# Optimization experiments

Measured on AMD Instinct MI355X. Metric: run time of the kernel, lower is better.

Reference implementation:

```python
import jax, jax.numpy as jnp
import numpy as np

FOCAL_ALPHA = 0.25
FOCAL_GAMMA = 2.0
IOU_POS_THRESH = 0.5


def setup_inputs() -> dict:
    A, G, C = 262144, 256, 80
    key = jax.random.key(0)
    k = jax.random.split(key, 8)
    # anchors: random boxes with centers in [0,1024], sizes in [16,128]
    actr = jax.random.uniform(k[0], (A, 2), minval=0.0, maxval=1024.0)
    awh = jax.random.uniform(k[1], (A, 2), minval=16.0, maxval=128.0)
    anchors = jnp.concatenate([actr - 0.5 * awh, actr + 0.5 * awh], axis=1)
    # ground-truth boxes: sizes in [32,256]
    gctr = jax.random.uniform(k[2], (G, 2), minval=0.0, maxval=1024.0)
    gwh = jax.random.uniform(k[3], (G, 2), minval=32.0, maxval=256.0)
    gt_boxes = jnp.concatenate([gctr - 0.5 * gwh, gctr + 0.5 * gwh], axis=1)
    cls_logits = jax.random.normal(k[4], (A, C), dtype=jnp.float32)
    # small deltas so exp(delta * width) in this module's decode stays finite
    bbox_reg = jax.random.normal(k[5], (A, 4), dtype=jnp.float32) * 0.02
    centerness = jax.random.normal(k[6], (A,), dtype=jnp.float32)
    gt_labels = jax.random.randint(k[7], (G,), 0, C, dtype=jnp.int32)
    return {"anchors": anchors, "cls_logits": cls_logits, "bbox_reg": bbox_reg,
            "centerness": centerness, "gt_boxes": gt_boxes, "gt_labels": gt_labels}


def _compute_loss(anchors, cls_logits, bbox_reg, centerness, gt_boxes, gt_labels):
    A, C = cls_logits.shape
    f32 = cls_logits.dtype
    # ---- box_iou: [A, G] pairwise IoU ----
    area_a = (anchors[:, 2] - anchors[:, 0]) * (anchors[:, 3] - anchors[:, 1])
    area_g = (gt_boxes[:, 2] - gt_boxes[:, 0]) * (gt_boxes[:, 3] - gt_boxes[:, 1])
    lt = jnp.maximum(anchors[:, None, :2], gt_boxes[None, :, :2])
    rb = jnp.minimum(anchors[:, None, 2:], gt_boxes[None, :, 2:])
    wh = jnp.maximum(rb - lt, 0.0)
    inter = wh[..., 0] * wh[..., 1]
    iou = inter / (area_a[:, None] + area_g[None, :] - inter)
    max_iou = iou.max(axis=1)
    midx = iou.argmax(axis=1)
    pos = max_iou > IOU_POS_THRESH
    posf = pos.astype(f32)
    npos = posf.sum()
    denom = jnp.maximum(npos, 1.0)
    mboxes = gt_boxes[midx]            # [A,4] matched GT box per anchor
    mlabels = gt_labels[midx]          # [A]
    # ---- focal loss over ALL anchors (targets = -1 for negatives) ----
    cls_t = jnp.where(pos, mlabels, -1)
    logp = jax.nn.log_softmax(cls_logits, axis=-1)
    # torch gathers class index; -1 wraps to last class (python-style indexing)
    ce = -jnp.take_along_axis(logp, (cls_t % C)[:, None], axis=1)[:, 0]
    p = jnp.exp(-ce)
    fl = (1.0 - p) ** FOCAL_GAMMA * ce
    af = jnp.where(cls_t == 1, FOCAL_ALPHA, 1.0 - FOCAL_ALPHA)
    cls_loss = (af * fl).mean()
    # ---- decode boxes (module's unusual parameterization: exp(delta*width)*width) ----
    w = anchors[:, 2] - anchors[:, 0]
    h = anchors[:, 3] - anchors[:, 1]
    cx = anchors[:, 0] + 0.5 * w
    cy = anchors[:, 1] + 0.5 * h
    pcx = cx + bbox_reg[:, 0] * w
    pcy = cy + bbox_reg[:, 1] * h
    pw = jnp.exp(bbox_reg[:, 2] * w) * w
    ph = jnp.exp(bbox_reg[:, 3] * h) * h
    pred = jnp.stack([pcx - 0.5 * pw, pcy - 0.5 * ph, pcx + 0.5 * pw, pcy + 0.5 * ph], axis=1)
    # ---- paired GIoU (diag of generalized_box_iou(pred, matched)) ----
    lt2 = jnp.maximum(pred[:, :2], mboxes[:, :2])
    rb2 = jnp.minimum(pred[:, 2:], mboxes[:, 2:])
    wh2 = jnp.maximum(rb2 - lt2, 0.0)
    inter2 = wh2[:, 0] * wh2[:, 1]
    area_p = (pred[:, 2] - pred[:, 0]) * (pred[:, 3] - pred[:, 1])
    area_m = (mboxes[:, 2] - mboxes[:, 0]) * (mboxes[:, 3] - mboxes[:, 1])
    union = area_p + area_m - inter2
    iou2 = inter2 / union
    el = jnp.minimum(pred[:, :2], mboxes[:, :2])
    er = jnp.maximum(pred[:, 2:], mboxes[:, 2:])
    ewh = jnp.maximum(er - el, 0.0)
    earea = ewh[:, 0] * ewh[:, 1]
    giou = iou2 - (earea - union) / earea
    reg_loss = 1.0 - (posf * giou).sum() / denom
    # ---- centerness targets + BCE-with-logits over positives ----
    lr = mboxes[:, jnp.array([0, 2])] - anchors[:, jnp.array([0, 2])]
    tb = mboxes[:, jnp.array([1, 3])] - anchors[:, jnp.array([1, 3])]
    lrmax = lr.max(axis=1)
    tbmax = tb.max(axis=1)
    r_lr = jnp.maximum(lr.min(axis=1) / jnp.where(lrmax == 0, 1.0, lrmax), 0.0)
    r_tb = jnp.maximum(tb.min(axis=1) / jnp.where(tbmax == 0, 1.0, tbmax), 0.0)
    ctr_t = jnp.sqrt(jnp.maximum(r_lr * r_tb, 1e-12))
    bce = jnp.logaddexp(0.0, centerness) - centerness * ctr_t
    ctr_loss = (posf * bce).sum() / denom
    # original skips the level entirely when there are no positives
    has = (npos > 0).astype(f32)
    cls_loss = cls_loss * has
    reg_loss = reg_loss * has
    ctr_loss = ctr_loss * has
    total = cls_loss + reg_loss + ctr_loss
    return total, cls_loss, reg_loss, ctr_loss


def reference(anchors, cls_logits, bbox_reg, centerness, gt_boxes, gt_labels):
    return _compute_loss(anchors, cls_logits, bbox_reg, centerness, gt_boxes, gt_labels)
```

## Files before the change

### kernel.cpp

```cpp
#include <hip/hip_runtime.h>
#include <math.h>

#define BLOCK 256
#define C_CLS 80
#define G_MAX 256
#define NCELL1 32
#define NCELLS (NCELL1 * NCELL1)
#define CAP 96
#define NBKT 256

static __device__ inline float frcp(float x) { return __builtin_amdgcn_rcpf(x); }

static __device__ inline int cell_of(float4 ab) {
    const float cx = 0.5f * (ab.x + ab.z);
    const float cy = 0.5f * (ab.y + ab.w);
    int ix = (int)(cx * (1.0f / 32.0f));
    int iy = (int)(cy * (1.0f / 32.0f));
    ix = ix < 0 ? 0 : (ix > NCELL1 - 1 ? NCELL1 - 1 : ix);
    iy = iy < 0 ? 0 : (iy > NCELL1 - 1 ? NCELL1 - 1 : iy);
    return iy * NCELL1 + ix;
}


__global__ __launch_bounds__(256) void k_build(
    const float4* __restrict__ gt, const int* __restrict__ gl,
    float* __restrict__ bsums, int* __restrict__ cnts,
    float4* __restrict__ boxes, int* __restrict__ labs, int G)
{
    __shared__ int s_wcnt[4];
    const int cell = blockIdx.x;
    const int ix = cell & (NCELL1 - 1), iy = cell >> 5;
    const float Dx1 = 32.0f * ix - 64.0f, Dx2 = 32.0f * ix + 96.0f;
    const float Dy1 = 32.0f * iy - 64.0f, Dy2 = 32.0f * iy + 96.0f;

    const int tid = threadIdx.x, wid = tid >> 6, lane = tid & 63;
    if (cell < NBKT && tid < 4) bsums[cell * 4 + tid] = 0.0f;

    bool keep = false;
    float4 g = make_float4(0.f, 0.f, 0.f, 0.f);
    int lb = 0;
    if (tid < G) {
        g = gt[tid];
        keep = (g.x <= Dx2) && (g.z >= Dx1) && (g.y <= Dy2) && (g.w >= Dy1);
        lb = gl[tid];
    }
    const unsigned long long mk = __ballot(keep);
    if (lane == 0) s_wcnt[wid] = __popcll(mk);
    __syncthreads();
    int prefix = 0;
    for (int w = 0; w < wid; ++w) prefix += s_wcnt[w];
    if (keep) {
        const int p = prefix + __popcll(mk & ((1ull << lane) - 1ull));
        if (p < CAP) {
            boxes[(size_t)cell * CAP + p] = g;
            labs[(size_t)cell * CAP + p] = lb;
        }
    }
    const int tot = s_wcnt[0] + s_wcnt[1] + s_wcnt[2] + s_wcnt[3];
    if (tot <= CAP) {
        const float4 sent = make_float4(1e30f, 1e30f, 1e30f, 1e30f);
        for (int p = tot + tid; p < CAP; p += 256) {
            boxes[(size_t)cell * CAP + p] = sent;
            labs[(size_t)cell * CAP + p] = 0;
        }
    }
    if (tid == 0) cnts[cell] = (tot > CAP) ? (1 << 30) : tot;
}

__global__ __launch_bounds__(BLOCK) void k_main(
    const float* __restrict__ anchors, const float* __restrict__ cls_logits,
    const float* __restrict__ bbox_reg, const float* __restrict__ centerness,
    const float* __restrict__ gt_boxes, const int* __restrict__ gt_labels,
    const int* __restrict__ cnts, const float4* __restrict__ boxes,
    const int* __restrict__ labs,
    float* __restrict__ bsums, int A, int G)
{
    const int tid = threadIdx.x;
    const int a = blockIdx.x * BLOCK + tid;
    const bool valid = a < A;

    float4 ab = make_float4(0.f, 0.f, 0.f, 0.f);
    if (valid) ab = reinterpret_cast<const float4*>(anchors)[a];
    const float area_a = (ab.z - ab.x) * (ab.w - ab.y);

    const int cell = cell_of(ab);
    const int cnt = valid ? cnts[cell] : 0;
    const bool big = cnt > CAP;
    const int c2 = big ? 0 : cnt;

    int wmax = c2;
    #pragma unroll
    for (int off = 1; off < 64; off <<= 1)
        wmax = max(wmax, __shfl_xor(wmax, off, 64));
    const int nch = (wmax + 7) >> 3;

    const float4* __restrict__ bl = boxes + (size_t)cell * CAP;
    float best = -1.0f;
    int bestk = 0, bidx = 0;
    float4 bA[8], bB[8];

    #define LOADCH(BUF, CH) { _Pragma("unroll")                                 \
        for (int u = 0; u < 8; ++u) BUF[u] = bl[(CH) * 8 + u]; }
    #define PROCCH(BUF, CH) { _Pragma("unroll")                                 \
        for (int u = 0; u < 8; ++u) {                                           \
            const float4 g = BUF[u];                                            \
            const float ga = (g.z - g.x) * (g.w - g.y);                         \
            const float lx = fmaxf(ab.x, g.x);                                  \
            const float ly = fmaxf(ab.y, g.y);                                  \
            const float rx = fminf(ab.z, g.z);                                  \
            const float ry = fminf(ab.w, g.w);                                  \
            const float iw = fmaxf(rx - lx, 0.0f);                              \
            const float ih = fmaxf(ry - ly, 0.0f);                              \
            const float inter = iw * ih;                                        \
            const float iou = inter * frcp(area_a + ga - inter);                \
            if (iou > best) { best = iou; bestk = (CH) * 8 + u; }               \
        } }

    if (nch > 0)  LOADCH(bA, 0)
    if (nch > 1)  LOADCH(bB, 1)
    if (nch > 0)  PROCCH(bA, 0)
    if (nch > 2)  LOADCH(bA, 2)
    if (nch > 1)  PROCCH(bB, 1)
    if (nch > 3)  LOADCH(bB, 3)
    if (nch > 2)  PROCCH(bA, 2)
    if (nch > 4)  LOADCH(bA, 4)
    if (nch > 3)  PROCCH(bB, 3)
    if (nch > 5)  LOADCH(bB, 5)
    if (nch > 4)  PROCCH(bA, 4)
    if (nch > 6)  LOADCH(bA, 6)
    if (nch > 5)  PROCCH(bB, 5)
    if (nch > 7)  LOADCH(bB, 7)
    if (nch > 6)  PROCCH(bA, 6)
    if (nch > 8)  LOADCH(bA, 8)
    if (nch > 7)  PROCCH(bB, 7)
    if (nch > 9)  LOADCH(bB, 9)
    if (nch > 8)  PROCCH(bA, 8)
    if (nch > 10) LOADCH(bA, 10)
    if (nch > 9)  PROCCH(bB, 9)
    if (nch > 11) LOADCH(bB, 11)
    if (nch > 10) PROCCH(bA, 10)
    if (nch > 11) PROCCH(bB, 11)
    #undef LOADCH
    #undef PROCCH

    if (__ballot(big) != 0ull) {
        if (big) {
            best = -1.0f; bidx = 0;
            for (int j = 0; j < G; ++j) {
                const float4 g = reinterpret_cast<const float4*>(gt_boxes)[j];
                const float ga = (g.z - g.x) * (g.w - g.y);
                const float lx = fmaxf(ab.x, g.x);
                const float ly = fmaxf(ab.y, g.y);
                const float rx = fminf(ab.z, g.z);
                const float ry = fminf(ab.w, g.w);
                const float iw = fmaxf(rx - lx, 0.0f);
                const float ih = fmaxf(ry - ly, 0.0f);
                const float inter = iw * ih;
                const float iou = inter * frcp(area_a + ga - inter);
                if (iou > best) { best = iou; bidx = j; }
            }
        }
    }

    float c_affl = 0.f, c_pos = 0.f, c_giou = 0.f, c_bce = 0.f;

    if (valid) {
        const bool pos = best > 0.5f;
        int lab = -1;
        float4 mb = make_float4(0.f, 0.f, 0.f, 0.f);
        if (pos) {
            if (big) { mb = reinterpret_cast<const float4*>(gt_boxes)[bidx]; lab = gt_labels[bidx]; }
            else     { mb = bl[bestk]; lab = labs[(size_t)cell * CAP + bestk]; }
        }

        const float4* row4 = reinterpret_cast<const float4*>(cls_logits + (size_t)a * C_CLS);
        float4 rr[C_CLS / 4];
        #pragma unroll
        for (int k = 0; k < C_CLS / 4; ++k) rr[k] = row4[k];

        float m = -3.4e38f;
        #pragma unroll
        for (int k = 0; k < C_CLS / 4; ++k) {
            const float4 v = rr[k];
            m = fmaxf(m, fmaxf(fmaxf(v.x, v.y), fmaxf(v.z, v.w)));
        }
        float s = 0.0f;
        #pragma unroll
        for (int k = 0; k < C_CLS / 4; ++k) {
            const float4 v = rr[k];
            s += __expf(v.x - m) + __expf(v.y - m)
               + __expf(v.z - m) + __expf(v.w - m);
        }
        const float v79 = rr[C_CLS / 4 - 1].w;
        const float lse = m + __logf(s);
        const float l_idx = pos ? cls_logits[(size_t)a * C_CLS + lab] : v79;
        const float ce = lse - l_idx;
        const float p  = __expf(-ce);
        const float om = 1.0f - p;
        const float fl = om * om * ce;
        const float af = (pos && lab == 1) ? 0.25f : 0.75f;
        c_affl = af * fl;

        if (pos) {
            const float w  = ab.z - ab.x;
            const float h  = ab.w - ab.y;
            const float cx = ab.x + 0.5f * w;
            const float cy = ab.y + 0.5f * h;
            const float4 t = reinterpret_cast<const float4*>(bbox_reg)[a];
            const float pcx = cx + t.x * w;
            const float pcy = cy + t.y * h;
            const float pw  = __expf(t.z * w) * w;
            const float ph  = __expf(t.w * h) * h;
            const float p0 = pcx - 0.5f * pw;
            const float p1 = pcy - 0.5f * ph;
            const float p2 = pcx + 0.5f * pw;
            const float p3 = pcy + 0.5f * ph;

            const float lx2 = fmaxf(p0, mb.x);
            const float ly2 = fmaxf(p1, mb.y);
            const float rx2 = fminf(p2, mb.z);
            const float ry2 = fminf(p3, mb.w);
            const float iw2 = fmaxf(rx2 - lx2, 0.0f);
            const float ih2 = fmaxf(ry2 - ly2, 0.0f);
            const float inter2 = iw2 * ih2;
            const float area_p = (p2 - p0) * (p3 - p1);
            const float area_m = (mb.z - mb.x) * (mb.w - mb.y);
            const float uni = area_p + area_m - inter2;
            const float iou2 = inter2 * frcp(uni);
            const float elx = fminf(p0, mb.x);
            const float ely = fminf(p1, mb.y);
            const float erx = fmaxf(p2, mb.z);
            const float ery = fmaxf(p3, mb.w);
            const float ew = fmaxf(erx - elx, 0.0f);
            const float eh = fmaxf(ery - ely, 0.0f);
            const float earea = ew * eh;
            const float giou = iou2 - (earea - uni) * frcp(earea);
            c_giou = giou;

            const float lr0 = mb.x - ab.x;
            const float lr1 = mb.z - ab.z;
            const float tb0 = mb.y - ab.y;
            const float tb1 = mb.w - ab.w;
            const float lrmax = fmaxf(lr0, lr1);
            const float lrmin = fminf(lr0, lr1);
            const float tbmax = fmaxf(tb0, tb1);
            const float tbmin = fminf(tb0, tb1);
            const float r_lr = fmaxf(lrmin * frcp(lrmax == 0.0f ? 1.0f : lrmax), 0.0f);
            const float r_tb = fmaxf(tbmin * frcp(tbmax == 0.0f ? 1.0f : tbmax), 0.0f);
            const float ctr_t = sqrtf(fmaxf(r_lr * r_tb, 1e-12f));
            const float c = centerness[a];
            const float bce = fmaxf(c, 0.0f) + log1pf(__expf(-fabsf(c))) - c * ctr_t;
            c_bce = bce;
            c_pos = 1.0f;
        }
    }

    __shared__ float red[4][BLOCK / 64];
    float vals[4] = { c_affl, c_pos, c_giou, c_bce };
    #pragma unroll
    for (int i = 0; i < 4; ++i) {
        float v = vals[i];
        #pragma unroll
        for (int off = 32; off > 0; off >>= 1) v += __shfl_down(v, off, 64);
        if ((tid & 63) == 0) red[i][tid >> 6] = v;
    }
    __syncthreads();
    if (tid < 4) {
        float v = 0.f;
        #pragma unroll
        for (int wv = 0; wv < BLOCK / 64; ++wv) v += red[tid][wv];
        atomicAdd(&bsums[(blockIdx.x & (NBKT - 1)) * 4 + tid], v);
    }
}

__global__ __launch_bounds__(BLOCK) void detloss_fallback(
    const float* __restrict__ anchors, const float* __restrict__ cls_logits,
    const float* __restrict__ bbox_reg, const float* __restrict__ centerness,
    const float* __restrict__ gt_boxes, const int* __restrict__ gt_labels,
    float* __restrict__ bsums, int A, int G)
{
    __shared__ float4 s_gt[G_MAX];
    __shared__ float  s_ga[G_MAX];
    __shared__ int    s_gl[G_MAX];
    const int tid = threadIdx.x;
    for (int j = tid; j < G; j += BLOCK) {
        float4 g = reinterpret_cast<const float4*>(gt_boxes)[j];
        s_gt[j] = g;
        s_ga[j] = (g.z - g.x) * (g.w - g.y);
        s_gl[j] = gt_labels[j];
    }
    __syncthreads();
    const int a = blockIdx.x * BLOCK + tid;
    float c_affl = 0.f, c_pos = 0.f, c_giou = 0.f, c_bce = 0.f;
    if (a < A) {
        const float4 ab = reinterpret_cast<const float4*>(anchors)[a];
        const float area_a = (ab.z - ab.x) * (ab.w - ab.y);
        float best = -1.0f; int bidx = 0;
        for (int j = 0; j < G; ++j) {
            const float4 g = s_gt[j];
            const float lx = fmaxf(ab.x, g.x), ly = fmaxf(ab.y, g.y);
            const float rx = fminf(ab.z, g.z), ry = fminf(ab.w, g.w);
            const float iw = fmaxf(rx - lx, 0.0f), ih = fmaxf(ry - ly, 0.0f);
            const float inter = iw * ih;
            const float iou = inter * frcp(area_a + s_ga[j] - inter);
            if (iou > best) { best = iou; bidx = j; }
        }
        const bool pos = best > 0.5f;
        const float posf = pos ? 1.0f : 0.0f;
        const float4 mb = s_gt[bidx];
        const int mlab = s_gl[bidx];
        const float4* row4 = reinterpret_cast<const float4*>(cls_logits + (size_t)a * C_CLS);
        float m = -3.4e38f, s = 0.0f, v79 = 0.0f;
        #pragma unroll
        for (int k = 0; k < C_CLS / 4; ++k) {
            const float4 v = row4[k];
            const float m4 = fmaxf(fmaxf(v.x, v.y), fmaxf(v.z, v.w));
            const float mn = fmaxf(m, m4);
            s = s * __expf(m - mn) + __expf(v.x - mn) + __expf(v.y - mn)
              + __expf(v.z - mn) + __expf(v.w - mn);
            m = mn;
            if (k == C_CLS / 4 - 1) v79 = v.w;
        }
        const float lse = m + __logf(s);
        const float l_idx = pos ? cls_logits[(size_t)a * C_CLS + mlab] : v79;
        const float ce = lse - l_idx;
        const float p = __expf(-ce);
        const float om = 1.0f - p;
        const float fl = om * om * ce;
        const float af = (pos && mlab == 1) ? 0.25f : 0.75f;
        c_affl = af * fl;
        const float w = ab.z - ab.x, h = ab.w - ab.y;
        const float cx = ab.x + 0.5f * w, cy = ab.y + 0.5f * h;
        const float4 t = reinterpret_cast<const float4*>(bbox_reg)[a];
        const float pcx = cx + t.x * w, pcy = cy + t.y * h;
        const float pw = __expf(t.z * w) * w, ph = __expf(t.w * h) * h;
        const float p0 = pcx - 0.5f * pw, p1 = pcy - 0.5f * ph;
        const float p2 = pcx + 0.5f * pw, p3 = pcy + 0.5f * ph;
        const float lx2 = fmaxf(p0, mb.x), ly2 = fmaxf(p1, mb.y);
        const float rx2 = fminf(p2, mb.z), ry2 = fminf(p3, mb.w);
        const float iw2 = fmaxf(rx2 - lx2, 0.0f), ih2 = fmaxf(ry2 - ly2, 0.0f);
        const float inter2 = iw2 * ih2;
        const float area_p = (p2 - p0) * (p3 - p1);
        const float area_m = (mb.z - mb.x) * (mb.w - mb.y);
        const float uni = area_p + area_m - inter2;
        const float iou2 = inter2 * frcp(uni);
        const float elx = fminf(p0, mb.x), ely = fminf(p1, mb.y);
        const float erx = fmaxf(p2, mb.z), ery = fmaxf(p3, mb.w);
        const float ew = fmaxf(erx - elx, 0.0f), eh = fmaxf(ery - ely, 0.0f);
        const float earea = ew * eh;
        const float giou = iou2 - (earea - uni) * frcp(earea);
        c_giou = posf * giou;
        const float lr0 = mb.x - ab.x, lr1 = mb.z - ab.z;
        const float tb0 = mb.y - ab.y, tb1 = mb.w - ab.w;
        const float lrmax = fmaxf(lr0, lr1), lrmin = fminf(lr0, lr1);
        const float tbmax = fmaxf(tb0, tb1), tbmin = fminf(tb0, tb1);
        const float r_lr = fmaxf(lrmin * frcp(lrmax == 0.0f ? 1.0f : lrmax), 0.0f);
        const float r_tb = fmaxf(tbmin * frcp(tbmax == 0.0f ? 1.0f : tbmax), 0.0f);
        const float ctr_t = sqrtf(fmaxf(r_lr * r_tb, 1e-12f));
        const float c = centerness[a];
        const float bce = fmaxf(c, 0.0f) + log1pf(__expf(-fabsf(c))) - c * ctr_t;
        c_bce = posf * bce;
        c_pos = posf;
    }
    __shared__ float red[4][BLOCK / 64];
    float vals[4] = { c_affl, c_pos, c_giou, c_bce };
    #pragma unroll
    for (int i = 0; i < 4; ++i) {
        float v = vals[i];
        #pragma unroll
        for (int off = 32; off > 0; off >>= 1) v += __shfl_down(v, off, 64);
        if ((tid & 63) == 0) red[i][tid >> 6] = v;
    }
    __syncthreads();
    if (tid < 4) {
        float v = 0.f;
        #pragma unroll
        for (int w = 0; w < BLOCK / 64; ++w) v += red[tid][w];
        atomicAdd(&bsums[(blockIdx.x & (NBKT - 1)) * 4 + tid], v);
    }
}

__global__ __launch_bounds__(NBKT) void detloss_final(
    const float* __restrict__ bsums, float* __restrict__ out, int A)
{
    const int t = threadIdx.x;
    float4 v = reinterpret_cast<const float4*>(bsums)[t];
    #pragma unroll
    for (int off = 32; off > 0; off >>= 1) {
        v.x += __shfl_down(v.x, off, 64);
        v.y += __shfl_down(v.y, off, 64);
        v.z += __shfl_down(v.z, off, 64);
        v.w += __shfl_down(v.w, off, 64);
    }
    __shared__ float4 r[NBKT / 64];
    if ((t & 63) == 0) r[t >> 6] = v;
    __syncthreads();
    if (t == 0) {
        float s_affl = 0.f, npos = 0.f, sgiou = 0.f, sbce = 0.f;
        #pragma unroll
        for (int w = 0; w < NBKT / 64; ++w) {
            s_affl += r[w].x; npos += r[w].y; sgiou += r[w].z; sbce += r[w].w;
        }
        float cls = s_affl / (float)A;
        const float denom = fmaxf(npos, 1.0f);
        float reg = 1.0f - sgiou / denom;
        float ctr = sbce / denom;
        const float has = (npos > 0.0f) ? 1.0f : 0.0f;
        cls *= has; reg *= has; ctr *= has;
        out[0] = cls + reg + ctr;
        out[1] = cls;
        out[2] = reg;
        out[3] = ctr;
    }
}

extern "C" void kernel_launch(void* const* d_in, const int* in_sizes, int n_in,
                              void* d_out, int out_size, void* d_ws, size_t ws_size,
                              hipStream_t stream) {
    const float* anchors    = (const float*)d_in[0];
    const float* cls_logits = (const float*)d_in[1];
    const float* bbox_reg   = (const float*)d_in[2];
    const float* centerness = (const float*)d_in[3];
    const float* gt_boxes   = (const float*)d_in[4];
    const int*   gt_labels  = (const int*)d_in[5];
    const int A = in_sizes[0] / 4;
    const int G = in_sizes[4] / 4;

    float* bsums = (float*)d_ws;
    const int grid = (A + BLOCK - 1) / BLOCK;

    const size_t need = (size_t)(4 * NBKT + NCELLS + (size_t)NCELLS * CAP * 4
                                 + (size_t)NCELLS * CAP) * 4;

    if (ws_size >= need && G <= 256) {
        int*    cnts  = (int*)d_ws + 4 * NBKT;
        float4* boxes = (float4*)((float*)d_ws + 4 * NBKT + NCELLS);
        int*    labs  = (int*)((float*)d_ws + 4 * NBKT + NCELLS + (size_t)NCELLS * CAP * 4);

        k_build<<<NCELLS, 256, 0, stream>>>((const float4*)gt_boxes, gt_labels,
                                            bsums, cnts, boxes, labs, G);
        k_main<<<grid, BLOCK, 0, stream>>>(anchors, cls_logits, bbox_reg,
                                           centerness, gt_boxes, gt_labels,
                                           cnts, boxes, labs, bsums, A, G);
    } else {
        const int Gc = G > G_MAX ? G_MAX : G;
        hipMemsetAsync(bsums, 0, 4 * NBKT * sizeof(float), stream);
        detloss_fallback<<<grid, BLOCK, 0, stream>>>(anchors, cls_logits, bbox_reg,
                                                     centerness, gt_boxes, gt_labels,
                                                     bsums, A, Gc);
    }
    detloss_final<<<1, NBKT, 0, stream>>>(bsums, (float*)d_out, A);
}
```

Before: 39.65 us.

## Split each anchor across two lanes for candidate IoU scan and softmax row

Each anchor is now handled by two lanes of a wavefront: the two halves interleave over the cell's candidate GT boxes in groups of four and merge their argmax with a cross-half shuffle. The 80-logit row is also split, so each lane loads 10 float4s and the max and sum are combined by shuffles. This halves per-thread register pressure (launch bounds now ask for 8 blocks) and serial IoU work, aiming for more memory parallelism and occupancy. The cost is twice as many threads and blocks, extra shuffles, and the upper half of each wavefront idling during the per-anchor loss tail.

```diff
diff --git a/kernel.cpp b/kernel.cpp
--- a/kernel.cpp
+++ b/kernel.cpp
@@ -67,42 +67,45 @@
     if (tid == 0) cnts[cell] = (tot > CAP) ? (1 << 30) : tot;
 }
 
-__global__ __launch_bounds__(BLOCK) void k_main(
-    const float* __restrict__ anchors, const float* __restrict__ cls_logits,
-    const float* __restrict__ bbox_reg, const float* __restrict__ centerness,
-    const float* __restrict__ gt_boxes, const int* __restrict__ gt_labels,
+__global__ __launch_bounds__(BLOCK, 8) void k_main(
+    const float4* __restrict__ anchors4, const float* __restrict__ cls_logits,
+    const float4* __restrict__ bbox_reg4, const float* __restrict__ centerness,
+    const float4* __restrict__ gt4, const int* __restrict__ gl,
     const int* __restrict__ cnts, const float4* __restrict__ boxes,
     const int* __restrict__ labs,
     float* __restrict__ bsums, int A, int G)
 {
-    const int tid = threadIdx.x;
-    const int a = blockIdx.x * BLOCK + tid;
+    const int tid  = threadIdx.x;
+    const int lane = tid & 63;
+    const int wv   = tid >> 6;
+    const int sub  = lane & 31;
+    const int half = lane >> 5;
+    const int a    = blockIdx.x * (BLOCK / 2) + wv * 32 + sub;
     const bool valid = a < A;
-
-    float4 ab = make_float4(0.f, 0.f, 0.f, 0.f);
-    if (valid) ab = reinterpret_cast<const float4*>(anchors)[a];
+    const int ar = valid ? a : 0;
+
+    const float4 ab = anchors4[ar];
     const float area_a = (ab.z - ab.x) * (ab.w - ab.y);
-
     const int cell = cell_of(ab);
-    const int cnt = valid ? cnts[cell] : 0;
-    const bool big = cnt > CAP;
-    const int c2 = big ? 0 : cnt;
+    const int cnt = cnts[cell];
+    const bool big = valid && (cnt > CAP);
+    const int c2 = (big || !valid) ? 0 : cnt;
 
     int wmax = c2;
     #pragma unroll
     for (int off = 1; off < 64; off <<= 1)
         wmax = max(wmax, __shfl_xor(wmax, off, 64));
-    const int nch = (wmax + 7) >> 3;
+    const int nq = (wmax + 3) >> 2;
 
     const float4* __restrict__ bl = boxes + (size_t)cell * CAP;
     float best = -1.0f;
-    int bestk = 0, bidx = 0;
-    float4 bA[8], bB[8];
-
-    #define LOADCH(BUF, CH) { _Pragma("unroll")                                 \
-        for (int u = 0; u < 8; ++u) BUF[u] = bl[(CH) * 8 + u]; }
-    #define PROCCH(BUF, CH) { _Pragma("unroll")                                 \
-        for (int u = 0; u < 8; ++u) {                                           \
+    int bestk = 0;
+    float4 qA[4], qB[4];
+
+    #define LOADQ(BUF, K) { _Pragma("unroll")                                   \
+        for (int u = 0; u < 4; ++u) BUF[u] = bl[(2*(K)+half)*4 + u]; }
+    #define PROCQ(BUF, K) { _Pragma("unroll")                                   \
+        for (int u = 0; u < 4; ++u) {                                           \
             const float4 g = BUF[u];                                            \
             const float ga = (g.z - g.x) * (g.w - g.y);                         \
             const float lx = fmaxf(ab.x, g.x);                                  \
@@ -113,41 +116,43 @@
             const float ih = fmaxf(ry - ly, 0.0f);                              \
             const float inter = iw * ih;                                        \
             const float iou = inter * frcp(area_a + ga - inter);                \
-            if (iou > best) { best = iou; bestk = (CH) * 8 + u; }               \
+            if (iou > best) { best = iou; bestk = (2*(K)+half)*4 + u; }         \
         } }
-
-    if (nch > 0)  LOADCH(bA, 0)
-    if (nch > 1)  LOADCH(bB, 1)
-    if (nch > 0)  PROCCH(bA, 0)
-    if (nch > 2)  LOADCH(bA, 2)
-    if (nch > 1)  PROCCH(bB, 1)
-    if (nch > 3)  LOADCH(bB, 3)
-    if (nch > 2)  PROCCH(bA, 2)
-    if (nch > 4)  LOADCH(bA, 4)
-    if (nch > 3)  PROCCH(bB, 3)
-    if (nch > 5)  LOADCH(bB, 5)
-    if (nch > 4)  PROCCH(bA, 4)
-    if (nch > 6)  LOADCH(bA, 6)
-    if (nch > 5)  PROCCH(bB, 5)
-    if (nch > 7)  LOADCH(bB, 7)
-    if (nch > 6)  PROCCH(bA, 6)
-    if (nch > 8)  LOADCH(bA, 8)
-    if (nch > 7)  PROCCH(bB, 7)
-    if (nch > 9)  LOADCH(bB, 9)
-    if (nch > 8)  PROCCH(bA, 8)
-    if (nch > 10) LOADCH(bA, 10)
-    if (nch > 9)  PROCCH(bB, 9)
-    if (nch > 11) LOADCH(bB, 11)
-    if (nch > 10) PROCCH(bA, 10)
-    if (nch > 11) PROCCH(bB, 11)
-    #undef LOADCH
-    #undef PROCCH
+    #define QON(K) (2*(K)+half < nq)
+
+    if (QON(0))  LOADQ(qA, 0)
+    if (QON(1))  LOADQ(qB, 1)
+    if (QON(0))  PROCQ(qA, 0)
+    if (QON(2))  LOADQ(qA, 2)
+    if (QON(1))  PROCQ(qB, 1)
+    if (QON(3))  LOADQ(qB, 3)
+    if (QON(2))  PROCQ(qA, 2)
+    if (QON(4))  LOADQ(qA, 4)
+    if (QON(3))  PROCQ(qB, 3)
+    if (QON(5))  LOADQ(qB, 5)
+    if (QON(4))  PROCQ(qA, 4)
+    if (QON(6))  LOADQ(qA, 6)
+    if (QON(5))  PROCQ(qB, 5)
+    if (QON(7))  LOADQ(qB, 7)
+    if (QON(6))  PROCQ(qA, 6)
+    if (QON(8))  LOADQ(qA, 8)
+    if (QON(7))  PROCQ(qB, 7)
+    if (QON(9))  LOADQ(qB, 9)
+    if (QON(8))  PROCQ(qA, 8)
+    if (QON(10)) LOADQ(qA, 10)
+    if (QON(9))  PROCQ(qB, 9)
+    if (QON(11)) LOADQ(qB, 11)
+    if (QON(10)) PROCQ(qA, 10)
+    if (QON(11)) PROCQ(qB, 11)
+    #undef LOADQ
+    #undef PROCQ
+    #undef QON
 
     if (__ballot(big) != 0ull) {
         if (big) {
-            best = -1.0f; bidx = 0;
+            best = -1.0f; bestk = 0;
             for (int j = 0; j < G; ++j) {
-                const float4 g = reinterpret_cast<const float4*>(gt_boxes)[j];
+                const float4 g = gt4[j];
                 const float ga = (g.z - g.x) * (g.w - g.y);
                 const float lx = fmaxf(ab.x, g.x);
                 const float ly = fmaxf(ab.y, g.y);
@@ -157,43 +162,53 @@
                 const float ih = fmaxf(ry - ly, 0.0f);
                 const float inter = iw * ih;
                 const float iou = inter * frcp(area_a + ga - inter);
-                if (iou > best) { best = iou; bidx = j; }
+                if (iou > best) { best = iou; bestk = j; }
             }
         }
     }
 
+    {
+        const float ov = __shfl_xor(best, 32, 64);
+        const int   oi = __shfl_xor(bestk, 32, 64);
+        if (ov > best || (ov == best && oi < bestk)) { best = ov; bestk = oi; }
+    }
+
+    const float4* __restrict__ row4 =
+        reinterpret_cast<const float4*>(cls_logits + (size_t)ar * C_CLS) + 10 * half;
+    float4 rr[10];
+    #pragma unroll
+    for (int k = 0; k < 10; ++k) rr[k] = row4[k];
+
+    float lm = -3.4e38f;
+    #pragma unroll
+    for (int k = 0; k < 10; ++k) {
+        const float4 v = rr[k];
+        lm = fmaxf(lm, fmaxf(fmaxf(v.x, v.y), fmaxf(v.z, v.w)));
+    }
+    const float m = fmaxf(lm, __shfl_xor(lm, 32, 64));
+    float ls = 0.0f;
+    #pragma unroll
+    for (int k = 0; k < 10; ++k) {
+        const float4 v = rr[k];
+        ls += __expf(v.x - m) + __expf(v.y - m)
+            + __expf(v.z - m) + __expf(v.w - m);
+    }
+    const float s = ls + __shfl_xor(ls, 32, 64);
+    const float lse = m + __logf(s);
+    const float l_neg = __shfl(rr[9].w, sub | 32, 64);
+
+    const bool pos = valid && (best > 0.5f);
+
     float c_affl = 0.f, c_pos = 0.f, c_giou = 0.f, c_bce = 0.f;
-
-    if (valid) {
-        const bool pos = best > 0.5f;
+    if (half == 0 && valid) {
         int lab = -1;
+        float l_idx = l_neg;
         float4 mb = make_float4(0.f, 0.f, 0.f, 0.f);
         if (pos) {
-            if (big) { mb = reinterpret_cast<const float4*>(gt_boxes)[bidx]; lab = gt_labels[bidx]; }
+            if (big) { mb = gt4[bestk]; lab = gl[bestk]; }
             else     { mb = bl[bestk]; lab = labs[(size_t)cell * CAP + bestk]; }
-        }
-
-        const float4* row4 = reinterpret_cast<const float4*>(cls_logits + (size_t)a * C_CLS);
-        float4 rr[C_CLS / 4];
-        #pragma unroll
-        for (int k = 0; k < C_CLS / 4; ++k) rr[k] = row4[k];
-
-        float m = -3.4e38f;
-        #pragma unroll
-        for (int k = 0; k < C_CLS / 4; ++k) {
-            const float4 v = rr[k];
-            m = fmaxf(m, fmaxf(fmaxf(v.x, v.y), fmaxf(v.z, v.w)));
-        }
-        float s = 0.0f;
-        #pragma unroll
-        for (int k = 0; k < C_CLS / 4; ++k) {
-            const float4 v = rr[k];
-            s += __expf(v.x - m) + __expf(v.y - m)
-               + __expf(v.z - m) + __expf(v.w - m);
-        }
-        const float v79 = rr[C_CLS / 4 - 1].w;
-        const float lse = m + __logf(s);
-        const float l_idx = pos ? cls_logits[(size_t)a * C_CLS + lab] : v79;
+            l_idx = cls_logits[(size_t)a * C_CLS + lab];
+        }
         const float ce = lse - l_idx;
         const float p  = __expf(-ce);
         const float om = 1.0f - p;
@@ -206,7 +221,7 @@
             const float h  = ab.w - ab.y;
             const float cx = ab.x + 0.5f * w;
             const float cy = ab.y + 0.5f * h;
-            const float4 t = reinterpret_cast<const float4*>(bbox_reg)[a];
+            const float4 t = bbox_reg4[a];
             const float pcx = cx + t.x * w;
             const float pcy = cy + t.y * h;
             const float pw  = __expf(t.z * w) * w;
@@ -262,13 +277,13 @@
         float v = vals[i];
         #pragma unroll
         for (int off = 32; off > 0; off >>= 1) v += __shfl_down(v, off, 64);
-        if ((tid & 63) == 0) red[i][tid >> 6] = v;
+        if (lane == 0) red[i][wv] = v;
     }
     __syncthreads();
     if (tid < 4) {
         float v = 0.f;
         #pragma unroll
-        for (int wv = 0; wv < BLOCK / 64; ++wv) v += red[tid][wv];
+        for (int w = 0; w < BLOCK / 64; ++w) v += red[tid][w];
         atomicAdd(&bsums[(blockIdx.x & (NBKT - 1)) * 4 + tid], v);
     }
 }
@@ -427,7 +442,6 @@
     const int G = in_sizes[4] / 4;
 
     float* bsums = (float*)d_ws;
-    const int grid = (A + BLOCK - 1) / BLOCK;
 
     const size_t need = (size_t)(4 * NBKT + NCELLS + (size_t)NCELLS * CAP * 4
                                  + (size_t)NCELLS * CAP) * 4;
@@ -439,12 +453,15 @@
 
         k_build<<<NCELLS, 256, 0, stream>>>((const float4*)gt_boxes, gt_labels,
                                             bsums, cnts, boxes, labs, G);
-        k_main<<<grid, BLOCK, 0, stream>>>(anchors, cls_logits, bbox_reg,
-                                           centerness, gt_boxes, gt_labels,
-                                           cnts, boxes, labs, bsums, A, G);
+        const int grid2 = (A + BLOCK / 2 - 1) / (BLOCK / 2);
+        k_main<<<grid2, BLOCK, 0, stream>>>((const float4*)anchors, cls_logits,
+                                            (const float4*)bbox_reg, centerness,
+                                            (const float4*)gt_boxes, gt_labels,
+                                            cnts, boxes, labs, bsums, A, G);
     } else {
         const int Gc = G > G_MAX ? G_MAX : G;
         hipMemsetAsync(bsums, 0, 4 * NBKT * sizeof(float), stream);
+        const int grid = (A + BLOCK - 1) / BLOCK;
         detloss_fallback<<<grid, BLOCK, 0, stream>>>(anchors, cls_logits, bbox_reg,
                                                      centerness, gt_boxes, gt_labels,
                                                      bsums, A, Gc);
```

Measured after the change: 40.30 us. Within noise of the previous version (+1.6%).
